# Kernel tuning notes

Hardware: AMD Instinct MI355X
Metric: run time of the kernel (lower is better)

## Reference

```python
import jax, jax.numpy as jnp
import numpy as np

# Izhikevich params (regular spiking), Euler step with dt=1
A, B_P, C, D, V_TH, DT = 0.02, 0.2, -65.0, 8.0, 30.0, 1.0


def _izh_scan(currents):
    """Run an Izhikevich cell over time. currents: [T, B, F] -> spikes [T, B, F]."""
    shp = currents.shape[1:]
    v0 = jnp.full(shp, C, dtype=currents.dtype)
    u0 = jnp.full(shp, B_P * C, dtype=currents.dtype)

    def step(state, i_t):
        v, u = state
        v = v + DT * (0.04 * v * v + 5.0 * v + 140.0 - u + i_t)
        u = u + DT * A * (B_P * v - u)
        z = (v >= V_TH).astype(currents.dtype)  # spike (heaviside)
        v = jnp.where(z > 0, C, v)               # reset
        u = u + z * D
        return (v, u), z

    (vT, uT), spikes = jax.lax.scan(step, (v0, u0), currents)
    return spikes, (vT, uT)


def setup_inputs() -> dict:
    key = jax.random.key(0)
    k1, k2, k3, k4, k5 = jax.random.split(key, 5)
    T, B, F_IN, F_HID = 2048, 8192, 4, 2
    xs = jax.random.normal(k1, (T, B, F_IN), dtype=jnp.float32)
    # PyTorch Linear default init: U(-1/sqrt(fan_in), 1/sqrt(fan_in)); scaled normal is fine for a baseline
    W_in = jax.random.normal(k2, (F_HID, F_IN), dtype=jnp.float32) * 0.5
    b_in = jax.random.normal(k3, (F_HID,), dtype=jnp.float32) * 0.5
    W_out = jax.random.normal(k4, (1, F_HID), dtype=jnp.float32) * 0.5
    b_out = jax.random.normal(k5, (1,), dtype=jnp.float32) * 0.5
    return {"xs": xs, "W_in": W_in, "b_in": b_in, "W_out": W_out, "b_out": b_out}


def reference(xs, W_in, b_in, W_out, b_out):
    # input linear: [T,B,4] @ [4,2] -> [T,B,2]
    h = jnp.einsum('tbi,oi->tbo', xs, W_in) + b_in
    input_spikes, _ = _izh_scan(h)
    # output linear: [T,B,2] -> [T,B,1]
    y = jnp.einsum('tbi,oi->tbo', input_spikes, W_out) + b_out
    output_spikes, _ = _izh_scan(y)
    return output_spikes
```

## Files before the change

kernel.cpp:

```cpp
#include <hip/hip_runtime.h>

namespace {

constexpr int T   = 2048;
constexpr int B   = 8192;
constexpr int C   = 16;
constexpr int NCH = T / C;

__device__ __forceinline__ void barrier_nodrain() {
    asm volatile("s_waitcnt lgkmcnt(0)\n\ts_barrier" ::: "memory");
}

__device__ __forceinline__ bool izh_core(float& v, float& u, float I) {
#pragma clang fp contract(off)
    float m2 = (0.04f * v) * v;
    float s1 = m2 + (5.0f * v);
    float s2 = s1 + 140.0f;
    float s3 = s2 - u;
    float s4 = s3 + I;
    float vn = v + s4;
    float m4 = 0.2f * vn;
    float s5 = m4 - u;
    float un = u + 0.02f * s5;
    bool  sp = (vn >= 30.0f);
    v = sp ? -65.0f : vn;
    float d8 = sp ? 8.0f : 0.0f;
    u = un + d8;
    return sp;
}

__global__ __launch_bounds__(192, 1) void izh3(
    const float* __restrict__ xs,
    const float* __restrict__ W_in, const float* __restrict__ b_in,
    const float* __restrict__ W_out, const float* __restrict__ b_out,
    float* __restrict__ out)
{
#pragma clang fp contract(off)
    __shared__ float zbuf[2][2][C][64];
    const int lane = threadIdx.x & 63;
    const int wid  = threadIdx.x >> 6;
    const int b    = blockIdx.x * 64 + lane;

    float v = -65.0f, u = -13.0f;

    if (wid < 2) {
        const float wa = W_in[wid * 4 + 0], wb = W_in[wid * 4 + 1];
        const float wc = W_in[wid * 4 + 2], wd = W_in[wid * 4 + 3];
        const float bi = b_in[wid];
        const float4* xp = reinterpret_cast<const float4*>(xs) + b;

        float4 ring[C];
#pragma unroll
        for (int j = 0; j < C; ++j) ring[j] = xp[(size_t)j * B];

        for (int k = 0; k < NCH; ++k) {
            const float4* nxt = xp + (size_t)((k + 1) & (NCH - 1)) * C * B;
            const int p = k & 1;
#pragma unroll
            for (int j = 0; j < C; ++j) {
                const float4 x = ring[j];
                ring[j] = nxt[(size_t)j * B];
                float h = (((x.x * wa) + (x.y * wb)) + (x.z * wc)) + (x.w * wd);
                h = h + bi;
                bool sp = izh_core(v, u, h);
                zbuf[wid][p][j][lane] = sp ? 1.0f : 0.0f;
            }
            barrier_nodrain();
        }
    } else {
        const float wo0 = W_out[0], wo1 = W_out[1], bo = b_out[0];
        const float c00 = ((0.0f * wo0) + (0.0f * wo1)) + bo;
        const float c10 = ((1.0f * wo0) + (0.0f * wo1)) + bo;
        const float c01 = ((0.0f * wo0) + (1.0f * wo1)) + bo;
        const float c11 = ((1.0f * wo0) + (1.0f * wo1)) + bo;
        float* op = out + b;

        auto consume = [&](int kk) {
#pragma clang fp contract(off)
            const int p  = kk & 1;
            const int tb = kk * C;
#pragma unroll
            for (int j = 0; j < C; ++j) {
                float sp0 = zbuf[0][p][j][lane];
                float sp1 = zbuf[1][p][j][lane];
                float yt  = (sp1 != 0.0f) ? c11 : c10;
                float yf  = (sp1 != 0.0f) ? c01 : c00;
                float y   = (sp0 != 0.0f) ? yt : yf;
                bool spo  = izh_core(v, u, y);
                op[(size_t)(tb + j) * B] = spo ? 1.0f : 0.0f;
            }
        };

        for (int k = 0; k < NCH; ++k) {
            if (k > 0) consume(k - 1);
            barrier_nodrain();
        }
        consume(NCH - 1);
    }
}

}

extern "C" void kernel_launch(void* const* d_in, const int* in_sizes, int n_in,
                              void* d_out, int out_size, void* d_ws, size_t ws_size,
                              hipStream_t stream) {
    const float* xs    = (const float*)d_in[0];
    const float* W_in  = (const float*)d_in[1];
    const float* b_in  = (const float*)d_in[2];
    const float* W_out = (const float*)d_in[3];
    const float* b_out = (const float*)d_in[4];
    float* out = (float*)d_out;

    dim3 grid(B / 64), block(192);
    hipLaunchKernelGGL(izh3, grid, block, 0, stream,
                       xs, W_in, b_in, W_out, b_out, out);
}
```

Before: 437.9 us.

## Add dedicated loader waves computing input linear into LDS ring and restructure Izhikevich step

Adds two producer waves per block that load xs and compute both hidden input currents into a 4-slot LDS ring. This takes global loads and the input linear off the two recurrent waves, which now only read currents from LDS. The Izhikevich step is rewritten to compute the spike and no-spike candidates in parallel and select between them, shortening the serial dependency chain per timestep. The cost is a larger block (320 threads), more LDS, and an extra barrier-synchronized pipeline stage.

```diff
diff --git a/kernel.cpp b/kernel.cpp
--- a/kernel.cpp
+++ b/kernel.cpp
@@ -6,96 +6,140 @@
 constexpr int B   = 8192;
 constexpr int C   = 16;
 constexpr int NCH = T / C;
+constexpr int NB  = 4;
 
 __device__ __forceinline__ void barrier_nodrain() {
     asm volatile("s_waitcnt lgkmcnt(0)\n\ts_barrier" ::: "memory");
 }
 
-__device__ __forceinline__ bool izh_core(float& v, float& u, float I) {
+struct IzhState {
+    float vnp;
+    float up;
+    bool  spp;
+};
+
+__device__ __forceinline__ bool izh_step(IzhState& s, float I) {
 #pragma clang fp contract(off)
-    float m2 = (0.04f * v) * v;
-    float s1 = m2 + (5.0f * v);
-    float s2 = s1 + 140.0f;
-    float s3 = s2 - u;
-    float s4 = s3 + I;
-    float vn = v + s4;
-    float m4 = 0.2f * vn;
-    float s5 = m4 - u;
-    float un = u + 0.02f * s5;
-    bool  sp = (vn >= 30.0f);
-    v = sp ? -65.0f : vn;
-    float d8 = sp ? 8.0f : 0.0f;
-    u = un + d8;
+    const float K0 = ((0.04f * (-65.0f)) * (-65.0f) + (5.0f * (-65.0f))) + 140.0f;
+    float m2a = 0.04f * s.vnp;
+    float m2  = m2a * s.vnp;
+    float f5  = 5.0f * s.vnp;
+    float s2A = (m2 + f5) + 140.0f;
+    float s3A = s2A - s.up;
+    float s4A = s3A + I;
+    float vnA = s.vnp + s4A;
+    float s3S = K0 - s.up;
+    float s4S = s3S + I;
+    float vnS = (-65.0f) + s4S;
+    float vn  = s.spp ? vnS : vnA;
+    bool  sp  = (vn >= 30.0f);
+    float m4  = 0.2f * vn;
+    float s5  = m4 - s.up;
+    float tt  = 0.02f * s5;
+    float un  = s.up + tt;
+    float d8  = sp ? 8.0f : 0.0f;
+    s.up  = un + d8;
+    s.vnp = vn;
+    s.spp = sp;
     return sp;
 }
 
-__global__ __launch_bounds__(192, 1) void izh3(
+__global__ __launch_bounds__(320, 1) void izh5(
     const float* __restrict__ xs,
     const float* __restrict__ W_in, const float* __restrict__ b_in,
     const float* __restrict__ W_out, const float* __restrict__ b_out,
     float* __restrict__ out)
 {
-#pragma clang fp contract(off)
-    __shared__ float zbuf[2][2][C][64];
+    __shared__ float hbuf[2][NB][C][64];
+    __shared__ float sbuf[2][2][C][64];
+
     const int lane = threadIdx.x & 63;
     const int wid  = threadIdx.x >> 6;
     const int b    = blockIdx.x * 64 + lane;
 
-    float v = -65.0f, u = -13.0f;
-
-    if (wid < 2) {
-        const float wa = W_in[wid * 4 + 0], wb = W_in[wid * 4 + 1];
-        const float wc = W_in[wid * 4 + 2], wd = W_in[wid * 4 + 3];
-        const float bi = b_in[wid];
+    if (wid >= 3) {
+#pragma clang fp contract(off)
+        const int w = wid - 3;
+        const float w00 = W_in[0], w01 = W_in[1], w02 = W_in[2], w03 = W_in[3];
+        const float w10 = W_in[4], w11 = W_in[5], w12 = W_in[6], w13 = W_in[7];
+        const float bi0 = b_in[0], bi1 = b_in[1];
         const float4* xp = reinterpret_cast<const float4*>(xs) + b;
 
-        float4 ring[C];
+        auto fill = [&](int m) {
+#pragma clang fp contract(off)
+            const int slot = m & (NB - 1);
+            float4 xv[C];
 #pragma unroll
-        for (int j = 0; j < C; ++j) ring[j] = xp[(size_t)j * B];
-
-        for (int k = 0; k < NCH; ++k) {
-            const float4* nxt = xp + (size_t)((k + 1) & (NCH - 1)) * C * B;
-            const int p = k & 1;
+            for (int j = 0; j < C; ++j) xv[j] = xp[(size_t)(m * C + j) * B];
 #pragma unroll
             for (int j = 0; j < C; ++j) {
-                const float4 x = ring[j];
-                ring[j] = nxt[(size_t)j * B];
-                float h = (((x.x * wa) + (x.y * wb)) + (x.z * wc)) + (x.w * wd);
-                h = h + bi;
-                bool sp = izh_core(v, u, h);
-                zbuf[wid][p][j][lane] = sp ? 1.0f : 0.0f;
+                const float4 x = xv[j];
+                float h0 = (((x.x * w00) + (x.y * w01)) + (x.z * w02)) + (x.w * w03);
+                h0 = h0 + bi0;
+                float h1 = (((x.x * w10) + (x.y * w11)) + (x.z * w12)) + (x.w * w13);
+                h1 = h1 + bi1;
+                hbuf[0][slot][j][lane] = h0;
+                hbuf[1][slot][j][lane] = h1;
+            }
+        };
+
+        fill(w);
+        barrier_nodrain();
+        for (int r = 0; r <= NCH; ++r) {
+            const int m = r + 2;
+            if (m < NCH && (m & 1) == w) fill(m);
+            barrier_nodrain();
+        }
+    } else if (wid < 2) {
+#pragma clang fp contract(off)
+        IzhState st{-65.0f, -13.0f, true};
+        barrier_nodrain();
+        for (int r = 0; r <= NCH; ++r) {
+            if (r < NCH) {
+                const int slot = r & (NB - 1);
+                const int par  = r & 1;
+                float Iv[C];
+#pragma unroll
+                for (int j = 0; j < C; ++j) Iv[j] = hbuf[wid][slot][j][lane];
+#pragma unroll
+                for (int j = 0; j < C; ++j) {
+                    bool sp = izh_step(st, Iv[j]);
+                    sbuf[wid][par][j][lane] = sp ? 1.0f : 0.0f;
+                }
             }
             barrier_nodrain();
         }
     } else {
+#pragma clang fp contract(off)
         const float wo0 = W_out[0], wo1 = W_out[1], bo = b_out[0];
         const float c00 = ((0.0f * wo0) + (0.0f * wo1)) + bo;
         const float c10 = ((1.0f * wo0) + (0.0f * wo1)) + bo;
         const float c01 = ((0.0f * wo0) + (1.0f * wo1)) + bo;
         const float c11 = ((1.0f * wo0) + (1.0f * wo1)) + bo;
         float* op = out + b;
-
-        auto consume = [&](int kk) {
-#pragma clang fp contract(off)
-            const int p  = kk & 1;
-            const int tb = kk * C;
+        IzhState st{-65.0f, -13.0f, true};
+        barrier_nodrain();
+        for (int r = 0; r <= NCH; ++r) {
+            if (r >= 1) {
+                const int c   = r - 1;
+                const int par = c & 1;
+                float z0[C], z1[C];
 #pragma unroll
-            for (int j = 0; j < C; ++j) {
-                float sp0 = zbuf[0][p][j][lane];
-                float sp1 = zbuf[1][p][j][lane];
-                float yt  = (sp1 != 0.0f) ? c11 : c10;
-                float yf  = (sp1 != 0.0f) ? c01 : c00;
-                float y   = (sp0 != 0.0f) ? yt : yf;
-                bool spo  = izh_core(v, u, y);
-                op[(size_t)(tb + j) * B] = spo ? 1.0f : 0.0f;
+                for (int j = 0; j < C; ++j) {
+                    z0[j] = sbuf[0][par][j][lane];
+                    z1[j] = sbuf[1][par][j][lane];
+                }
+#pragma unroll
+                for (int j = 0; j < C; ++j) {
+                    float yt = (z1[j] != 0.0f) ? c11 : c10;
+                    float yf = (z1[j] != 0.0f) ? c01 : c00;
+                    float y  = (z0[j] != 0.0f) ? yt : yf;
+                    bool spo = izh_step(st, y);
+                    op[(size_t)(c * C + j) * B] = spo ? 1.0f : 0.0f;
+                }
             }
-        };
-
-        for (int k = 0; k < NCH; ++k) {
-            if (k > 0) consume(k - 1);
             barrier_nodrain();
         }
-        consume(NCH - 1);
     }
 }
 
@@ -111,7 +155,7 @@
     const float* b_out = (const float*)d_in[4];
     float* out = (float*)d_out;
 
-    dim3 grid(B / 64), block(192);
-    hipLaunchKernelGGL(izh3, grid, block, 0, stream,
+    dim3 grid(B / 64), block(320);
+    hipLaunchKernelGGL(izh5, grid, block, 0, stream,
                        xs, W_in, b_in, W_out, b_out, out);
 }
```

Result: no change. 445.3 us (+1.7%).
